# Performance work log

Measured on AMD Instinct MI355X. Metric: run time of the kernel, lower is better.

The kernel has to match this reference:

```python
import math
import jax, jax.numpy as jnp
import numpy as np

B, N, D = 8, 2048, 512


def setup_inputs() -> dict:
    key = jax.random.key(0)
    ks = jax.random.split(key, 9)
    s = 1.0 / math.sqrt(D)
    return {
        "x": jax.random.normal(ks[0], (B, N, D), dtype=jnp.float32),
        "adj": jax.random.uniform(ks[1], (B, N, N), dtype=jnp.float32),
        "Wqk": jax.random.normal(ks[2], (D, D), dtype=jnp.float32) * s,
        "bqk": jax.random.normal(ks[3], (D,), dtype=jnp.float32) * s,
        "Wl": jax.random.normal(ks[4], (D, D), dtype=jnp.float32) * s,
        "bl": jax.random.normal(ks[5], (D,), dtype=jnp.float32) * s,
        "Wr": jax.random.normal(ks[6], (D, D), dtype=jnp.float32) * s,
        "Wd": jax.random.normal(ks[7], (D, 1), dtype=jnp.float32),
        "bd": jax.random.normal(ks[8], (D,), dtype=jnp.float32),
    }


def reference(x, adj, Wqk, bqk, Wl, bl, Wr, Wd, bd):
    # degree gating: sigmoid(Linear(rowsum(adj)))
    deg = jnp.sum(adj, axis=-1, keepdims=True)           # [B, N, 1]
    gate = jax.nn.sigmoid(deg * Wd[:, 0] + bd)           # [B, N, D]
    xg = x * gate
    # sigmoid QK features
    QK = jax.nn.sigmoid(xg @ Wqk.T + bqk)                # [B, N, D]
    scores = jnp.einsum("bnd,bmd->bnm", QK, QK) / math.sqrt(D)
    scores = scores * adj                                # adjacency mask
    attn = scores / (jnp.sum(scores, axis=-1, keepdims=True) + 1e-6)
    out = jnp.einsum("bnm,bmd->bnd", attn, xg)           # aggregate values
    out = out @ Wl.T + bl + xg @ Wr.T                    # left + right branch
    return jax.nn.relu(out)
```

## Files before the change

### kernel.cpp

```cpp
#include <hip/hip_runtime.h>
#include <hip/hip_bf16.h>


typedef __bf16 bf16;
typedef __bf16 bf16x8 __attribute__((ext_vector_type(8)));
typedef float  f32x4  __attribute__((ext_vector_type(4)));

#define Bb 8
#define Nn 2048
#define Dd 512

__device__ __forceinline__ bf16 to_bf16(float f) { return (bf16)f; }
__device__ __forceinline__ float sigmoidf_(float x) { return 1.0f / (1.0f + __expf(-x)); }

__device__ __forceinline__ void gld16(const void* g, void* l) {
    __builtin_amdgcn_global_load_lds(
        (__attribute__((address_space(1))) void*)(void*)g,
        (__attribute__((address_space(3))) void*)l,
        16, 0, 0);
}

__device__ __forceinline__ void gemm_bt_core(
    const bf16* __restrict__ A, const bf16* __restrict__ Bt,
    int lda, int ldb, int K,
    char* As, char* Bs, f32x4 acc[4][4])
{
    const int tid  = threadIdx.x;
    const int lane = tid & 63;
    const int wave = tid >> 6;
    const int wm = (wave >> 1) << 6;
    const int wn = (wave & 1) << 6;

    for (int kt = 0; kt < K; kt += 64) {
#pragma unroll
        for (int i = 0; i < 4; ++i) {
            int ff   = i * 256 + tid;
            int row  = ff >> 3;
            int slot = ff & 7;
            int gch  = slot ^ (row & 7);
            gld16(A  + (size_t)row * lda + kt + gch * 8, As + ff * 16);
            gld16(Bt + (size_t)row * ldb + kt + gch * 8, Bs + ff * 16);
        }
        __syncthreads();
#pragma unroll
        for (int ks = 0; ks < 2; ++ks) {
            bf16x8 af[4], bfr[4];
#pragma unroll
            for (int mi = 0; mi < 4; ++mi) {
                int row  = wm + mi * 16 + (lane & 15);
                int slot = ((ks << 2) + (lane >> 4)) ^ (row & 7);
                af[mi] = *(const bf16x8*)(As + row * 128 + slot * 16);
            }
#pragma unroll
            for (int ni = 0; ni < 4; ++ni) {
                int row  = wn + ni * 16 + (lane & 15);
                int slot = ((ks << 2) + (lane >> 4)) ^ (row & 7);
                bfr[ni] = *(const bf16x8*)(Bs + row * 128 + slot * 16);
            }
#pragma unroll
            for (int mi = 0; mi < 4; ++mi)
#pragma unroll
                for (int ni = 0; ni < 4; ++ni)
                    acc[mi][ni] = __builtin_amdgcn_mfma_f32_16x16x32_bf16(
                        af[mi], bfr[ni], acc[mi][ni], 0, 0, 0);
        }
        __syncthreads();
    }
}

#define GEMM_PROLOGUE()                                  \
    __shared__ __align__(16) char As[16384];             \
    __shared__ __align__(16) char Bs[16384];             \
    f32x4 acc[4][4];                                     \
    _Pragma("unroll") for (int mi = 0; mi < 4; ++mi)     \
    _Pragma("unroll") for (int ni = 0; ni < 4; ++ni)     \
        acc[mi][ni] = (f32x4){0.f, 0.f, 0.f, 0.f};

#define GEMM_EPILOGUE_BEGIN()                            \
    const int lane = threadIdx.x & 63;                   \
    const int wave = threadIdx.x >> 6;                   \
    const int wm = (wave >> 1) << 6;                     \
    const int wn = (wave & 1) << 6;                      \
    const int cq = lane >> 4;                            \
    const int cl = lane & 15;                            \
    _Pragma("unroll") for (int mi = 0; mi < 4; ++mi)     \
    _Pragma("unroll") for (int ni = 0; ni < 4; ++ni)     \
    _Pragma("unroll") for (int r = 0; r < 4; ++r) {      \
        const int row = blockRow + wm + mi * 16 + cq * 4 + r; \
        const int col = blockCol + wn + ni * 16 + cl;    \
        float v = acc[mi][ni][r];

#define GEMM_EPILOGUE_END() }

__global__ __launch_bounds__(256) void k_castw(
    const float* __restrict__ Wqk, const float* __restrict__ Wl,
    const float* __restrict__ Wr,
    bf16* __restrict__ Wqkb, bf16* __restrict__ Wlb, bf16* __restrict__ Wrb)
{
    int i = blockIdx.x * 256 + threadIdx.x;
    Wqkb[i] = to_bf16(Wqk[i]);
    Wlb[i]  = to_bf16(Wl[i]);
    Wrb[i]  = to_bf16(Wr[i]);
}

__global__ __launch_bounds__(256) void k_gate(
    const float* __restrict__ x, const float* __restrict__ adj,
    const float* __restrict__ Wd, const float* __restrict__ bd,
    bf16* __restrict__ xg)
{
    const int rowg = blockIdx.x;
    const float4* arow = (const float4*)(adj + (size_t)rowg * Nn);
    float4 v0 = arow[threadIdx.x];
    float4 v1 = arow[threadIdx.x + 256];
    float s = v0.x + v0.y + v0.z + v0.w + v1.x + v1.y + v1.z + v1.w;
#pragma unroll
    for (int off = 32; off > 0; off >>= 1) s += __shfl_down(s, off, 64);
    __shared__ float red[4];
    if ((threadIdx.x & 63) == 0) red[threadIdx.x >> 6] = s;
    __syncthreads();
    const float deg = red[0] + red[1] + red[2] + red[3];
#pragma unroll
    for (int d = threadIdx.x; d < Dd; d += 256) {
        float g = sigmoidf_(deg * Wd[d] + bd[d]);
        xg[(size_t)rowg * Dd + d] = to_bf16(x[(size_t)rowg * Dd + d] * g);
    }
}

__global__ __launch_bounds__(256) void k_transpose(
    const bf16* __restrict__ xg, bf16* __restrict__ xgT)
{
    const int b = blockIdx.z, nt = blockIdx.y, dt = blockIdx.x;
    __shared__ bf16 tile[64][66];
    const int c = threadIdx.x & 63, r0 = threadIdx.x >> 6;
    const bf16* src = xg + ((size_t)b * Nn + nt * 64) * Dd + dt * 64;
#pragma unroll
    for (int i = 0; i < 16; ++i) {
        int r = i * 4 + r0;
        tile[r][c] = src[(size_t)r * Dd + c];
    }
    __syncthreads();
    bf16* dst = xgT + ((size_t)b * Dd + dt * 64) * Nn + nt * 64;
#pragma unroll
    for (int i = 0; i < 16; ++i) {
        int r = i * 4 + r0;
        dst[(size_t)r * Nn + c] = tile[c][r];
    }
}

__global__ __launch_bounds__(256) void k_qk_gemm(
    const bf16* __restrict__ xg, const bf16* __restrict__ Wqkb,
    const float* __restrict__ bqk, bf16* __restrict__ QK)
{
    const int blockRow = blockIdx.y * 128;
    const int blockCol = blockIdx.x * 128;
    GEMM_PROLOGUE();
    gemm_bt_core(xg + (size_t)blockRow * Dd, Wqkb + (size_t)blockCol * Dd,
                 Dd, Dd, Dd, As, Bs, acc);
    GEMM_EPILOGUE_BEGIN();
    QK[(size_t)row * Dd + col] = to_bf16(sigmoidf_(v + bqk[col]));
    GEMM_EPILOGUE_END();
}

__global__ __launch_bounds__(256) void k_s_gemm(
    const bf16* __restrict__ QK, const float* __restrict__ adj,
    bf16* __restrict__ S)
{
    const int b = blockIdx.z;
    const int blockRow = blockIdx.y * 128;
    const int blockCol = blockIdx.x * 128;
    const bf16* Qb = QK + (size_t)b * Nn * Dd;
    GEMM_PROLOGUE();
    gemm_bt_core(Qb + (size_t)blockRow * Dd, Qb + (size_t)blockCol * Dd,
                 Dd, Dd, Dd, As, Bs, acc);
    const float scale = 0.044194173824159216f;
    GEMM_EPILOGUE_BEGIN();
    float a = adj[((size_t)b * Nn + row) * Nn + col];
    S[((size_t)b * Nn + row) * Nn + col] = to_bf16(v * scale * a);
    GEMM_EPILOGUE_END();
}

__global__ __launch_bounds__(256) void k_denom(
    const bf16* __restrict__ S, float* __restrict__ denom)
{
    const int rowg = blockIdx.x;
    const bf16* p = S + (size_t)rowg * Nn;
    bf16x8 v = *(const bf16x8*)(p + threadIdx.x * 8);
    float s = 0.f;
#pragma unroll
    for (int j = 0; j < 8; ++j) s += (float)v[j];
#pragma unroll
    for (int off = 32; off > 0; off >>= 1) s += __shfl_down(s, off, 64);
    __shared__ float red[4];
    if ((threadIdx.x & 63) == 0) red[threadIdx.x >> 6] = s;
    __syncthreads();
    if (threadIdx.x == 0)
        denom[rowg] = red[0] + red[1] + red[2] + red[3] + 1e-6f;
}

__global__ __launch_bounds__(256) void k_h_gemm(
    const bf16* __restrict__ S, const bf16* __restrict__ xgT,
    const float* __restrict__ denom, bf16* __restrict__ h)
{
    const int b = blockIdx.z;
    const int blockRow = blockIdx.y * 128;
    const int blockCol = blockIdx.x * 128;
    GEMM_PROLOGUE();
    gemm_bt_core(S + ((size_t)b * Nn + blockRow) * Nn,
                 xgT + ((size_t)b * Dd + blockCol) * Nn,
                 Nn, Nn, Nn, As, Bs, acc);
    GEMM_EPILOGUE_BEGIN();
    float dn = denom[b * Nn + row];
    h[((size_t)b * Nn + row) * Dd + col] = to_bf16(v / dn);
    GEMM_EPILOGUE_END();
}

__global__ __launch_bounds__(256) void k_out_gemm(
    const bf16* __restrict__ h, const bf16* __restrict__ xg,
    const bf16* __restrict__ Wlb, const bf16* __restrict__ Wrb,
    const float* __restrict__ bl, float* __restrict__ out)
{
    const int blockRow = blockIdx.y * 128;
    const int blockCol = blockIdx.x * 128;
    GEMM_PROLOGUE();
    gemm_bt_core(h  + (size_t)blockRow * Dd, Wlb + (size_t)blockCol * Dd,
                 Dd, Dd, Dd, As, Bs, acc);
    gemm_bt_core(xg + (size_t)blockRow * Dd, Wrb + (size_t)blockCol * Dd,
                 Dd, Dd, Dd, As, Bs, acc);
    GEMM_EPILOGUE_BEGIN();
    float o = v + bl[col];
    out[(size_t)row * Dd + col] = fmaxf(o, 0.f);
    GEMM_EPILOGUE_END();
}

extern "C" void kernel_launch(void* const* d_in, const int* in_sizes, int n_in,
                              void* d_out, int out_size, void* d_ws, size_t ws_size,
                              hipStream_t stream) {
    const float* x   = (const float*)d_in[0];
    const float* adj = (const float*)d_in[1];
    const float* Wqk = (const float*)d_in[2];
    const float* bqk = (const float*)d_in[3];
    const float* Wl  = (const float*)d_in[4];
    const float* bl  = (const float*)d_in[5];
    const float* Wr  = (const float*)d_in[6];
    const float* Wd  = (const float*)d_in[7];
    const float* bd  = (const float*)d_in[8];
    float* out = (float*)d_out;

    char* ws = (char*)d_ws;
    bf16* xg   = (bf16*)ws;  ws += (size_t)Bb * Nn * Dd * 2;
    bf16* xgT  = (bf16*)ws;  ws += (size_t)Bb * Dd * Nn * 2;
    bf16* QK   = (bf16*)ws;  ws += (size_t)Bb * Nn * Dd * 2;
    bf16* S    = (bf16*)ws;  ws += (size_t)Bb * Nn * Nn * 2;
    bf16* Wqkb = (bf16*)ws;  ws += (size_t)Dd * Dd * 2;
    bf16* Wlb  = (bf16*)ws;  ws += (size_t)Dd * Dd * 2;
    bf16* Wrb  = (bf16*)ws;  ws += (size_t)Dd * Dd * 2;
    float* denom = (float*)ws; ws += (size_t)Bb * Nn * 4;
    bf16* h = QK;

    k_castw<<<dim3(1024), 256, 0, stream>>>(Wqk, Wl, Wr, Wqkb, Wlb, Wrb);
    k_gate<<<dim3(Bb * Nn), 256, 0, stream>>>(x, adj, Wd, bd, xg);
    k_transpose<<<dim3(Dd / 64, Nn / 64, Bb), 256, 0, stream>>>(xg, xgT);
    k_qk_gemm<<<dim3(Dd / 128, (Bb * Nn) / 128), 256, 0, stream>>>(xg, Wqkb, bqk, QK);
    k_s_gemm<<<dim3(Nn / 128, Nn / 128, Bb), 256, 0, stream>>>(QK, adj, S);
    k_denom<<<dim3(Bb * Nn), 256, 0, stream>>>(S, denom);
    k_h_gemm<<<dim3(Dd / 128, Nn / 128, Bb), 256, 0, stream>>>(S, xgT, denom, h);
    k_out_gemm<<<dim3(Dd / 128, (Bb * Nn) / 128), 256, 0, stream>>>(h, xg, Wlb, Wrb, bl, out);
}
```

Measured before the change: 406.3 us.

## Stage GEMM epilogues through LDS for vectorized stores and fuse denominator via atomics

Every GEMM epilogue now writes its accumulators into shared memory in two half-tile phases, then reads them back row-contiguously. This lets global loads of adj and bias and the stores of S, QK, h and out use 16-byte vectors instead of scattered scalar accesses. The S-GEMM epilogue also computes partial row sums of the masked scores and atomically adds them into a zeroed denominator buffer, which removes the separate k_denom pass over S. The cost is extra LDS traffic and barriers per tile, plus atomic contention and an added memset.

```diff
diff --git a/kernel.cpp b/kernel.cpp
--- a/kernel.cpp
+++ b/kernel.cpp
@@ -9,6 +9,7 @@
 #define Bb 8
 #define Nn 2048
 #define Dd 512
+#define SMEM_BYTES 33792
 
 __device__ __forceinline__ bf16 to_bf16(float f) { return (bf16)f; }
 __device__ __forceinline__ float sigmoidf_(float x) { return 1.0f / (1.0f + __expf(-x)); }
@@ -69,28 +70,53 @@
 }
 
 #define GEMM_PROLOGUE()                                  \
-    __shared__ __align__(16) char As[16384];             \
-    __shared__ __align__(16) char Bs[16384];             \
+    __shared__ __align__(16) char smem[SMEM_BYTES];      \
+    char* As = smem;                                     \
+    char* Bs = smem + 16384;                             \
     f32x4 acc[4][4];                                     \
     _Pragma("unroll") for (int mi = 0; mi < 4; ++mi)     \
     _Pragma("unroll") for (int ni = 0; ni < 4; ++ni)     \
         acc[mi][ni] = (f32x4){0.f, 0.f, 0.f, 0.f};
 
-#define GEMM_EPILOGUE_BEGIN()                            \
-    const int lane = threadIdx.x & 63;                   \
-    const int wave = threadIdx.x >> 6;                   \
-    const int wm = (wave >> 1) << 6;                     \
-    const int wn = (wave & 1) << 6;                      \
-    const int cq = lane >> 4;                            \
-    const int cl = lane & 15;                            \
-    _Pragma("unroll") for (int mi = 0; mi < 4; ++mi)     \
-    _Pragma("unroll") for (int ni = 0; ni < 4; ++ni)     \
-    _Pragma("unroll") for (int r = 0; r < 4; ++r) {      \
-        const int row = blockRow + wm + mi * 16 + cq * 4 + r; \
-        const int col = blockCol + wn + ni * 16 + cl;    \
-        float v = acc[mi][ni][r];
-
-#define GEMM_EPILOGUE_END() }
+template <typename F>
+__device__ __forceinline__ void epilogue_rt(f32x4 acc[4][4], char* smem, F&& emit)
+{
+    const int tid  = threadIdx.x;
+    const int lane = tid & 63;
+    const int wave = tid >> 6;
+    const int wm = (wave >> 1) << 6;
+    const int wn = (wave & 1) << 6;
+    const int cq = lane >> 4;
+    const int cl = lane & 15;
+    float* t = (float*)smem;
+    const int chunk = tid & 15;
+    const int rbase = tid >> 4;
+#pragma unroll
+    for (int ph = 0; ph < 2; ++ph) {
+        __syncthreads();
+        if ((wm >> 6) == ph) {
+#pragma unroll
+            for (int mi = 0; mi < 4; ++mi)
+#pragma unroll
+                for (int ni = 0; ni < 4; ++ni)
+#pragma unroll
+                    for (int r = 0; r < 4; ++r) {
+                        int lr = mi * 16 + cq * 4 + r;
+                        int lc = wn + ni * 16 + cl;
+                        t[lr * 132 + lc] = acc[mi][ni][r];
+                    }
+        }
+        __syncthreads();
+#pragma unroll
+        for (int rr = 0; rr < 4; ++rr) {
+            int lr = rr * 16 + rbase;
+            f32x4 a = *(const f32x4*)&t[lr * 132 + chunk * 8];
+            f32x4 b = *(const f32x4*)&t[lr * 132 + chunk * 8 + 4];
+            float v[8] = {a[0], a[1], a[2], a[3], b[0], b[1], b[2], b[3]};
+            emit(ph * 64 + lr, chunk * 8, v);
+        }
+    }
+}
 
 __global__ __launch_bounds__(256) void k_castw(
     const float* __restrict__ Wqk, const float* __restrict__ Wl,
@@ -156,14 +182,21 @@
     GEMM_PROLOGUE();
     gemm_bt_core(xg + (size_t)blockRow * Dd, Wqkb + (size_t)blockCol * Dd,
                  Dd, Dd, Dd, As, Bs, acc);
-    GEMM_EPILOGUE_BEGIN();
-    QK[(size_t)row * Dd + col] = to_bf16(sigmoidf_(v + bqk[col]));
-    GEMM_EPILOGUE_END();
+    epilogue_rt(acc, smem, [&](int lr, int lc, float* v) {
+        int c = blockCol + lc;
+        float4 b0 = *(const float4*)(bqk + c);
+        float4 b1 = *(const float4*)(bqk + c + 4);
+        float bb[8] = {b0.x, b0.y, b0.z, b0.w, b1.x, b1.y, b1.z, b1.w};
+        bf16x8 o;
+#pragma unroll
+        for (int j = 0; j < 8; ++j) o[j] = to_bf16(sigmoidf_(v[j] + bb[j]));
+        *(bf16x8*)(QK + (size_t)(blockRow + lr) * Dd + c) = o;
+    });
 }
 
 __global__ __launch_bounds__(256) void k_s_gemm(
     const bf16* __restrict__ QK, const float* __restrict__ adj,
-    bf16* __restrict__ S)
+    bf16* __restrict__ S, float* __restrict__ denom)
 {
     const int b = blockIdx.z;
     const int blockRow = blockIdx.y * 128;
@@ -173,28 +206,26 @@
     gemm_bt_core(Qb + (size_t)blockRow * Dd, Qb + (size_t)blockCol * Dd,
                  Dd, Dd, Dd, As, Bs, acc);
     const float scale = 0.044194173824159216f;
-    GEMM_EPILOGUE_BEGIN();
-    float a = adj[((size_t)b * Nn + row) * Nn + col];
-    S[((size_t)b * Nn + row) * Nn + col] = to_bf16(v * scale * a);
-    GEMM_EPILOGUE_END();
-}
-
-__global__ __launch_bounds__(256) void k_denom(
-    const bf16* __restrict__ S, float* __restrict__ denom)
-{
-    const int rowg = blockIdx.x;
-    const bf16* p = S + (size_t)rowg * Nn;
-    bf16x8 v = *(const bf16x8*)(p + threadIdx.x * 8);
-    float s = 0.f;
-#pragma unroll
-    for (int j = 0; j < 8; ++j) s += (float)v[j];
-#pragma unroll
-    for (int off = 32; off > 0; off >>= 1) s += __shfl_down(s, off, 64);
-    __shared__ float red[4];
-    if ((threadIdx.x & 63) == 0) red[threadIdx.x >> 6] = s;
-    __syncthreads();
-    if (threadIdx.x == 0)
-        denom[rowg] = red[0] + red[1] + red[2] + red[3] + 1e-6f;
+    epilogue_rt(acc, smem, [&](int lr, int lc, float* v) {
+        int gRow = blockRow + lr;
+        size_t base = ((size_t)b * Nn + gRow) * Nn + blockCol + lc;
+        float4 a0 = *(const float4*)(adj + base);
+        float4 a1 = *(const float4*)(adj + base + 4);
+        float aa[8] = {a0.x, a0.y, a0.z, a0.w, a1.x, a1.y, a1.z, a1.w};
+        bf16x8 o;
+        float ds = 0.f;
+#pragma unroll
+        for (int j = 0; j < 8; ++j) {
+            float s = v[j] * scale * aa[j];
+            bf16 sb = to_bf16(s);
+            o[j] = sb;
+            ds += (float)sb;
+        }
+        *(bf16x8*)(S + base) = o;
+#pragma unroll
+        for (int off = 8; off > 0; off >>= 1) ds += __shfl_xor(ds, off, 16);
+        if ((threadIdx.x & 15) == 0) atomicAdd(&denom[b * Nn + gRow], ds);
+    });
 }
 
 __global__ __launch_bounds__(256) void k_h_gemm(
@@ -208,10 +239,14 @@
     gemm_bt_core(S + ((size_t)b * Nn + blockRow) * Nn,
                  xgT + ((size_t)b * Dd + blockCol) * Nn,
                  Nn, Nn, Nn, As, Bs, acc);
-    GEMM_EPILOGUE_BEGIN();
-    float dn = denom[b * Nn + row];
-    h[((size_t)b * Nn + row) * Dd + col] = to_bf16(v / dn);
-    GEMM_EPILOGUE_END();
+    epilogue_rt(acc, smem, [&](int lr, int lc, float* v) {
+        int gRow = blockRow + lr;
+        float inv = 1.0f / (denom[b * Nn + gRow] + 1e-6f);
+        bf16x8 o;
+#pragma unroll
+        for (int j = 0; j < 8; ++j) o[j] = to_bf16(v[j] * inv);
+        *(bf16x8*)(h + ((size_t)b * Nn + gRow) * Dd + blockCol + lc) = o;
+    });
 }
 
 __global__ __launch_bounds__(256) void k_out_gemm(
@@ -226,10 +261,20 @@
                  Dd, Dd, Dd, As, Bs, acc);
     gemm_bt_core(xg + (size_t)blockRow * Dd, Wrb + (size_t)blockCol * Dd,
                  Dd, Dd, Dd, As, Bs, acc);
-    GEMM_EPILOGUE_BEGIN();
-    float o = v + bl[col];
-    out[(size_t)row * Dd + col] = fmaxf(o, 0.f);
-    GEMM_EPILOGUE_END();
+    epilogue_rt(acc, smem, [&](int lr, int lc, float* v) {
+        int c = blockCol + lc;
+        float4 b0 = *(const float4*)(bl + c);
+        float4 b1 = *(const float4*)(bl + c + 4);
+        float bb[8] = {b0.x, b0.y, b0.z, b0.w, b1.x, b1.y, b1.z, b1.w};
+        float4 o0, o1;
+        o0.x = fmaxf(v[0] + bb[0], 0.f); o0.y = fmaxf(v[1] + bb[1], 0.f);
+        o0.z = fmaxf(v[2] + bb[2], 0.f); o0.w = fmaxf(v[3] + bb[3], 0.f);
+        o1.x = fmaxf(v[4] + bb[4], 0.f); o1.y = fmaxf(v[5] + bb[5], 0.f);
+        o1.z = fmaxf(v[6] + bb[6], 0.f); o1.w = fmaxf(v[7] + bb[7], 0.f);
+        float* p = out + (size_t)(blockRow + lr) * Dd + c;
+        *(float4*)p = o0;
+        *(float4*)(p + 4) = o1;
+    });
 }
 
 extern "C" void kernel_launch(void* const* d_in, const int* in_sizes, int n_in,
@@ -257,12 +302,12 @@
     float* denom = (float*)ws; ws += (size_t)Bb * Nn * 4;
     bf16* h = QK;
 
+    hipMemsetAsync(denom, 0, (size_t)Bb * Nn * sizeof(float), stream);
     k_castw<<<dim3(1024), 256, 0, stream>>>(Wqk, Wl, Wr, Wqkb, Wlb, Wrb);
     k_gate<<<dim3(Bb * Nn), 256, 0, stream>>>(x, adj, Wd, bd, xg);
     k_transpose<<<dim3(Dd / 64, Nn / 64, Bb), 256, 0, stream>>>(xg, xgT);
     k_qk_gemm<<<dim3(Dd / 128, (Bb * Nn) / 128), 256, 0, stream>>>(xg, Wqkb, bqk, QK);
-    k_s_gemm<<<dim3(Nn / 128, Nn / 128, Bb), 256, 0, stream>>>(QK, adj, S);
-    k_denom<<<dim3(Bb * Nn), 256, 0, stream>>>(S, denom);
+    k_s_gemm<<<dim3(Nn / 128, Nn / 128, Bb), 256, 0, stream>>>(QK, adj, S, denom);
     k_h_gemm<<<dim3(Dd / 128, Nn / 128, Bb), 256, 0, stream>>>(S, xgT, denom, h);
     k_out_gemm<<<dim3(Dd / 128, (Bb * Nn) / 128), 256, 0, stream>>>(h, xg, Wlb, Wrb, bl, out);
 }
```

Measured after the change: 404.6 us. Within noise of the previous version (-0.4%).
